# Kernel tuning notes

Measured on AMD Instinct MI355X. Metric: run time of the kernel, lower is better.

Reference implementation:

```python
import jax, jax.numpy as jnp
import numpy as np

D = 64      # in_features
U = 1024    # hidden units
B = 4096    # batch

def _build_masks():
    d0 = np.arange(D)
    dh = np.arange(U) % (D - 1)
    m0 = (d0[None, :] <= dh[:, None]).astype(np.float32)          # [U, D]
    m1 = (dh[None, :] <= dh[:, None]).astype(np.float32)          # [U, U]
    m2 = np.tile((dh[None, :] < d0[:, None]).astype(np.float32), (2, 1))  # [2D, U]
    return jnp.asarray(m0), jnp.asarray(m1), jnp.asarray(m2)


def setup_inputs() -> dict:
    key = jax.random.key(0)
    ks = jax.random.split(key, 7)
    scale = 0.02  # small init so exp(sigma) stays finite
    return {
        "u": jax.random.normal(ks[0], (B, D), dtype=jnp.float32),
        "W0": jax.random.normal(ks[1], (U, D), dtype=jnp.float32) * scale,
        "b0": jax.random.normal(ks[2], (U,), dtype=jnp.float32) * scale,
        "W1": jax.random.normal(ks[3], (U, U), dtype=jnp.float32) * scale,
        "b1": jax.random.normal(ks[4], (U,), dtype=jnp.float32) * scale,
        "W2": jax.random.normal(ks[5], (2 * D, U), dtype=jnp.float32) * scale,
        "b2": jax.random.normal(ks[6], (2 * D,), dtype=jnp.float32) * scale,
    }


def reference(u, W0, b0, W1, b1, W2, b2):
    m0, m1, m2 = _build_masks()
    mW0, mW1, mW2 = m0 * W0, m1 * W1, m2 * W2  # masked weights (constant across steps)

    def made(x):  # x: [B, D] -> mu, sigma each [B, D]
        h = jax.nn.relu(x @ mW0.T + b0)
        h = jax.nn.relu(h @ mW1.T + b1)
        z = h @ mW2.T + b2
        return z[:, :D], z[:, D:]

    def step(carry, i):
        x, ldj = carry
        mu, sigma = made(x)
        # ordering = arange(D) (sequential, not reversed) => idx == i
        x = x.at[:, i].set(u[:, i] * jnp.exp(sigma[:, i]) + mu[:, i])
        ldj = ldj.at[:, i].set(sigma[:, i])
        return (x, ldj), None

    x0 = jnp.zeros_like(u)
    ldj0 = jnp.zeros_like(u)
    (x, ldj), _ = jax.lax.scan(step, (x0, ldj0), jnp.arange(D))
    log_det_jacobian = jnp.sum(ldj, axis=1, keepdims=True)  # [B, 1]
    return x, log_det_jacobian
```

## Files before the change

### kernel.cpp

```cpp
#include <hip/hip_runtime.h>
#include <hip/hip_bf16.h>

#define BATCH 4096
#define NTHR 512

typedef __attribute__((ext_vector_type(8))) short bf16x8;
typedef __attribute__((ext_vector_type(4))) float f32x4;
typedef __attribute__((ext_vector_type(4))) short short4v;

#define BAR() asm volatile("s_waitcnt lgkmcnt(0)\n\ts_barrier" ::: "memory")

__host__ __device__ __forceinline__ int off1(int g) { return (g <= 16) ? 17 * g : 16 * g + 16; }
__host__ __device__ __forceinline__ int cntg(int g) { return (g < 16) ? 17 : 16; }
__host__ __device__ __forceinline__ int unitOf(int p) {
    int gp, jp;
    if (p < 272) { gp = p / 17; jp = p - gp * 17; }
    else         { gp = (p >> 4) - 1; jp = p & 15; }
    return gp + 63 * jp;
}
__device__ __forceinline__ short f2bf(float f) {
    __hip_bfloat16 h = __float2bfloat16(f);
    return *reinterpret_cast<short*>(&h);
}

__global__ void prep7(const float* __restrict__ W0, const float* __restrict__ b0,
                      const float* __restrict__ W1, const float* __restrict__ b1,
                      const float* __restrict__ W2,
                      short* __restrict__ W1f, short* __restrict__ W2f,
                      short* __restrict__ W0f, float* __restrict__ b1p) {
    __shared__ short ws[16][1032];
    const int b = blockIdx.x, t = threadIdx.x;
    if (b < 72) {
        const bool isW1 = (b < 64);
        const int n = t >> 5;
        int u;
        if (isW1) u = unitOf(b * 16 + n);
        else { const int c = b - 64; u = (n & 1) ? (64 + c * 8 + (n >> 1)) : (c * 8 + (n >> 1)); }
        const float* src = isW1 ? (W1 + (long)u * 1024) : (W2 + (long)u * 1024);
        const int c0 = (t & 31) * 4;
#pragma unroll
        for (int j = 0; j < 8; ++j) {
            int c = c0 + j * 128;
            float4 v = *(const float4*)&src[c];
            short4v sv;
            sv[0] = f2bf(v.x); sv[1] = f2bf(v.y); sv[2] = f2bf(v.z); sv[3] = f2bf(v.w);
            *(short4v*)&ws[n][c] = sv;
        }
        __syncthreads();
#pragma unroll 1
        for (int it = 0; it < 8; ++it) {
            int v = t + it * 512;
            if (v < 4032) {
                int g = v >> 6, lane2 = v & 63;
                int nn = lane2 & 15, aq2 = lane2 >> 4;
                bf16x8 pk;
#pragma unroll
                for (int e = 0; e < 8; ++e) {
                    int k = aq2 * 8 + e;
                    pk[e] = (k < cntg(g)) ? ws[nn][g + 63 * k] : (short)0;
                }
                if (isW1) *(bf16x8*)&W1f[(((long)g * 64 + b) * 64 + lane2) * 8] = pk;
                else      *(bf16x8*)&W2f[(((long)g * 8 + (b - 64)) * 64 + lane2) * 8] = pk;
            }
        }
    } else if (b < 88) {
        const int bb = b - 72;
#pragma unroll 1
        for (int j = 0; j < 16; ++j) {
            int q = t + j * 512;
            if (q < 8064) {
                int idx = bb * 8064 + q;
                int g = idx >> 11, rem = idx & 2047;
                int n2 = rem >> 10, kt = (rem >> 9) & 1, lane2 = (rem >> 3) & 63, e = rem & 7;
                int sl = n2 * 16 + (lane2 & 15);
                int kp = kt * 32 + ((lane2 >> 4) << 3) + e;
                float val = 0.f;
                if (sl < cntg(g)) {
                    int u = unitOf(off1(g) + sl);
                    if (kp == 0) val = b0[u];
                    else if (kp - 1 <= g) val = W0[u * 64 + kp - 1];
                }
                W0f[idx] = f2bf(val);
            }
        }
    } else {
        for (int p = t; p < 1024; p += 512) b1p[p] = b1[unitOf(p)];
    }
}

__global__ __launch_bounds__(NTHR, 2) void made7(
    const float* __restrict__ uin, const float* __restrict__ b2,
    const short* __restrict__ W1f, const short* __restrict__ W2f,
    const short* __restrict__ W0f, const float* __restrict__ b1p,
    float* __restrict__ out) {

    __shared__ __align__(16) short h1b[2][16][40];
    __shared__ __align__(16) short h2b[2][16][40];
    __shared__ __align__(16) short xhist[16][80];
    __shared__ __align__(16) float uT[64][16];
    __shared__ __align__(16) float xLs[16][68];
    __shared__ float ldjpart[8][16];

    const int t = threadIdx.x, lane = t & 63, wv = t >> 6;
    const int n = lane & 15, aq = lane >> 4;
    const int rowbase = blockIdx.x * 16;

    {
        int* z1 = (int*)&h1b[0][0][0];
        for (int idx = t; idx < 2 * 16 * 40 / 2; idx += NTHR) z1[idx] = 0;
        int* z2 = (int*)&h2b[0][0][0];
        for (int idx = t; idx < 2 * 16 * 40 / 2; idx += NTHR) z2[idx] = 0;
        int* z3 = (int*)&xhist[0][0];
        for (int idx = t; idx < 16 * 80 / 2; idx += NTHR) z3[idx] = 0;
    }
    if (t < 256) {
        int r = t >> 4, c0 = (t & 15) * 4;
        float4 v = *(const float4*)&uin[(long)(rowbase + r) * 64 + c0];
        uT[c0 + 0][r] = v.x; uT[c0 + 1][r] = v.y; uT[c0 + 2][r] = v.z; uT[c0 + 3][r] = v.w;
    }

    const int B = (wv == 0) ? 0 : (wv == 1) ? 7 : (wv == 2) ? 15 : 8 * wv;
    const int C = (wv == 1 || wv == 2) ? 9 : 8;

    f32x4 acc2[9];
#pragma unroll
    for (int s = 0; s < 9; ++s) {
        float bb = (s < C) ? b1p[(B + s) * 16 + n] : 0.f;
        acc2[s] = (f32x4){bb, bb, bb, bb};
    }
    f32x4 zacc;
    {
        int pc = wv * 16 + n;
        float bz = b2[(pc >> 1) + 64 * (pc & 1)];
        zacc = (f32x4){bz, bz, bz, bz};
    }

    bf16x8 w1f[9], w2g, w2gm1, w0f0, w0f1, w0f2;
#pragma unroll
    for (int s = 0; s < 9; ++s)
        if (s < C)
            w1f[s] = *(const bf16x8*)&W1f[(((long)0 * 64 + (B + s)) * 64 + lane) * 8];
    w2g = *(const bf16x8*)&W2f[(((long)0 * 8 + wv) * 64 + lane) * 8];
    w2gm1 = w2g;
    {
        const long gb = 8 * wv;
        w0f0 = *(const bf16x8*)&W0f[((gb * 4 + 0) * 64 + lane) * 8];
        w0f1 = *(const bf16x8*)&W0f[((gb * 4 + 1) * 64 + lane) * 8];
        w0f2 = *(const bf16x8*)&W0f[((gb * 4 + 2) * 64 + lane) * 8];
    }

    f32x4 ldjacc = {0.f, 0.f, 0.f, 0.f};
    BAR();
    if (t < 16) xhist[t][0] = (short)0x3F80;
    float ureg[4];
#pragma unroll
    for (int r = 0; r < 4; ++r) ureg[r] = uT[8 * wv + (n >> 1)][aq * 4 + r];

#pragma unroll 1
    for (int i = 0; i < 64; ++i) {
        const int g = i - 1;
        const bool isPub = (wv == (i >> 3));

        if (g >= 0) {
            const int og = off1(g);
            const int tf0 = og >> 4;
            const bf16x8 af1 = *(const bf16x8*)&h1b[(i + 1) & 1][n][aq * 8];
            const int s0 = tf0 - B;
#pragma unroll
            for (int s = 0; s < 9; ++s)
                if (s < C && s >= s0)
                    acc2[s] = __builtin_amdgcn_mfma_f32_16x16x32_bf16(af1, w1f[s], acc2[s], 0, 0, 0);
            {
                const int gp = (i < 63) ? i : 62;
                const int s0p = (off1(gp) >> 4) - B;
#pragma unroll
                for (int s = 0; s < 9; ++s)
                    if (s < C && s >= s0p)
                        w1f[s] = *(const bf16x8*)&W1f[(((long)gp * 64 + (B + s)) * 64 + lane) * 8];
            }
            const bool freshedPrev = (wv == ((i - 1) >> 3));
            if (!isPub && !freshedPrev && g >= 1) {
                const bf16x8 af2p = *(const bf16x8*)&h2b[(i - 1) & 1][n][aq * 8];
                zacc = __builtin_amdgcn_mfma_f32_16x16x32_bf16(af2p, w2gm1, zacc, 0, 0, 0);
            }
        }

        if (isPub) {
            if (g >= 0) {
                const int og = off1(g), cg = cntg(g);
                const int tf0 = og >> 4, tfl = (og + cg - 1) >> 4;
                if ((i & 7) == 0 && g >= 1) {
                    const bf16x8 af2p = *(const bf16x8*)&h2b[(i - 1) & 1][n][aq * 8];
                    zacc = __builtin_amdgcn_mfma_f32_16x16x32_bf16(af2p, w2gm1, zacc, 0, 0, 0);
                }
                {
                    const int sT = tf0 - B;
                    const int j = tf0 * 16 + n - og;
                    if (j >= 0 && j < cg) {
#pragma unroll
                        for (int r = 0; r < 4; ++r) {
                            float v = acc2[sT][r];
                            h2b[i & 1][aq * 4 + r][j] = f2bf(v > 0.f ? v : 0.f);
                        }
                    }
                }
                if (tfl != tf0) {
                    const int sT = tfl - B;
                    const int j = tfl * 16 + n - og;
                    if (j < cg) {
#pragma unroll
                        for (int r = 0; r < 4; ++r) {
                            float v = acc2[sT][r];
                            h2b[i & 1][aq * 4 + r][j] = f2bf(v > 0.f ? v : 0.f);
                        }
                    }
                }
                if ((g == 16 || g == 17) && n == 0) {
#pragma unroll
                    for (int r = 0; r < 4; ++r) h2b[i & 1][aq * 4 + r][16] = 0;
                }
                const bf16x8 af2 = *(const bf16x8*)&h2b[i & 1][n][aq * 8];
                zacc = __builtin_amdgcn_mfma_f32_16x16x32_bf16(af2, w2g, zacc, 0, 0, 0);
            }
            {
                const int n0 = 2 * (i & 7);
                f32x4 sgv;
#pragma unroll
                for (int r = 0; r < 4; ++r) sgv[r] = __shfl_xor(zacc[r], 1);
                if (n == n0) {
#pragma unroll
                    for (int r = 0; r < 4; ++r) {
                        const float sg = sgv[r], mu = zacc[r];
                        const float x = ureg[r] * __expf(sg) + mu;
                        ldjacc[r] += sg;
                        const int m = aq * 4 + r;
                        xLs[m][i] = x;
                        if (i < 63) xhist[m][i + 1] = f2bf(x);
                    }
                }
            }
            if (i < 63) {
                const bf16x8 ax0 = *(const bf16x8*)&xhist[n][aq * 8];
                f32x4 d0 = {0.f, 0.f, 0.f, 0.f};
                d0 = __builtin_amdgcn_mfma_f32_16x16x32_bf16(ax0, w0f0, d0, 0, 0, 0);
                if (i >= 31) {
                    const bf16x8 ax1 = *(const bf16x8*)&xhist[n][32 + aq * 8];
                    d0 = __builtin_amdgcn_mfma_f32_16x16x32_bf16(ax1, w0f1, d0, 0, 0, 0);
                }
                f32x4 d1 = {0.f, 0.f, 0.f, 0.f};
                if (i < 16)
                    d1 = __builtin_amdgcn_mfma_f32_16x16x32_bf16(ax0, w0f2, d1, 0, 0, 0);
#pragma unroll
                for (int r = 0; r < 4; ++r) {
                    float v = d0[r];
                    h1b[i & 1][aq * 4 + r][n] = f2bf(v > 0.f ? v : 0.f);
                }
                if (n == 0) {
#pragma unroll
                    for (int r = 0; r < 4; ++r) {
                        float v = (i < 16) ? (d1[r] > 0.f ? d1[r] : 0.f) : 0.f;
                        h1b[i & 1][aq * 4 + r][16] = f2bf(v);
                    }
                }
                if (i + 1 < 63 && ((i + 1) >> 3) == wv) {
                    const long gb = i + 1;
                    w0f0 = *(const bf16x8*)&W0f[((gb * 4 + 0) * 64 + lane) * 8];
                    w0f1 = *(const bf16x8*)&W0f[((gb * 4 + 1) * 64 + lane) * 8];
                    w0f2 = *(const bf16x8*)&W0f[((gb * 4 + 2) * 64 + lane) * 8];
                }
            }
        }

        w2gm1 = w2g;
        {
            const int gz = (i < 63) ? i : 62;
            w2g = *(const bf16x8*)&W2f[(((long)gz * 8 + wv) * 64 + lane) * 8];
        }
        BAR();
    }

#pragma unroll
    for (int r = 0; r < 4; ++r) {
        float v = ldjacc[r];
        v += __shfl_xor(v, 2);
        v += __shfl_xor(v, 4);
        v += __shfl_xor(v, 8);
        if (n == 0) ldjpart[wv][aq * 4 + r] = v;
    }
    BAR();

    if (t < 256) {
        int r = t >> 4, c = (t & 15) * 4;
        float4 v;
        v.x = xLs[r][c]; v.y = xLs[r][c + 1]; v.z = xLs[r][c + 2]; v.w = xLs[r][c + 3];
        *(float4*)&out[(long)(rowbase + r) * 64 + c] = v;
    }
    if (t < 16) {
        float s = 0.f;
#pragma unroll
        for (int w = 0; w < 8; ++w) s += ldjpart[w][t];
        out[(long)BATCH * 64 + rowbase + t] = s;
    }
}

extern "C" void kernel_launch(void* const* d_in, const int* in_sizes, int n_in,
                              void* d_out, int out_size, void* d_ws, size_t ws_size,
                              hipStream_t stream) {
    (void)in_sizes; (void)n_in; (void)out_size; (void)ws_size;
    const float* u  = (const float*)d_in[0];
    const float* W0 = (const float*)d_in[1];
    const float* b0 = (const float*)d_in[2];
    const float* W1 = (const float*)d_in[3];
    const float* b1 = (const float*)d_in[4];
    const float* W2 = (const float*)d_in[5];
    const float* b2 = (const float*)d_in[6];
    float* out = (float*)d_out;

    short* W1f = (short*)d_ws;
    short* W2f = (short*)((char*)d_ws + 4128768);
    short* W0f = (short*)((char*)d_ws + 4128768 + 516096);
    float* b1p = (float*)((char*)d_ws + 4128768 + 516096 + 258048);

    prep7<<<dim3(89), dim3(512), 0, stream>>>(W0, b0, W1, b1, W2, W1f, W2f, W0f, b1p);
    made7<<<dim3(BATCH / 16), dim3(NTHR), 0, stream>>>(u, b2, W1f, W2f, W0f, b1p, out);
}
```

Before: 212.6 us.

## Defer bulk MFMA accumulation by several steps and barrier every fourth iteration

The per-step layer-1 and layer-2 history buffers become 8-slot rings. Non-publishing waves now accumulate contributions several steps late, while the publishing wave patches in the most recent few steps itself with extra MFMAs using freshly loaded weight shards. This lets the block-wide barrier run only every fourth step instead of every step, cutting synchronisation on the serial 64-step chain. The cost is redundant MFMAs and extra weight loads on the critical wave, more LDS, and dropping the occupancy hint from launch_bounds.

```diff
diff --git a/kernel.cpp b/kernel.cpp
--- a/kernel.cpp
+++ b/kernel.cpp
@@ -23,7 +23,7 @@
     return *reinterpret_cast<short*>(&h);
 }
 
-__global__ void prep7(const float* __restrict__ W0, const float* __restrict__ b0,
+__global__ void prep9(const float* __restrict__ W0, const float* __restrict__ b0,
                       const float* __restrict__ W1, const float* __restrict__ b1,
                       const float* __restrict__ W2,
                       short* __restrict__ W1f, short* __restrict__ W2f,
@@ -88,14 +88,14 @@
     }
 }
 
-__global__ __launch_bounds__(NTHR, 2) void made7(
+__global__ __launch_bounds__(NTHR) void made9(
     const float* __restrict__ uin, const float* __restrict__ b2,
     const short* __restrict__ W1f, const short* __restrict__ W2f,
     const short* __restrict__ W0f, const float* __restrict__ b1p,
     float* __restrict__ out) {
 
-    __shared__ __align__(16) short h1b[2][16][40];
-    __shared__ __align__(16) short h2b[2][16][40];
+    __shared__ __align__(16) short h1r[8][16][40];
+    __shared__ __align__(16) short h2r[8][16][40];
     __shared__ __align__(16) short xhist[16][80];
     __shared__ __align__(16) float uT[64][16];
     __shared__ __align__(16) float xLs[16][68];
@@ -106,10 +106,10 @@
     const int rowbase = blockIdx.x * 16;
 
     {
-        int* z1 = (int*)&h1b[0][0][0];
-        for (int idx = t; idx < 2 * 16 * 40 / 2; idx += NTHR) z1[idx] = 0;
-        int* z2 = (int*)&h2b[0][0][0];
-        for (int idx = t; idx < 2 * 16 * 40 / 2; idx += NTHR) z2[idx] = 0;
+        int* z1 = (int*)&h1r[0][0][0];
+        for (int idx = t; idx < 8 * 16 * 40 / 2; idx += NTHR) z1[idx] = 0;
+        int* z2 = (int*)&h2r[0][0][0];
+        for (int idx = t; idx < 8 * 16 * 40 / 2; idx += NTHR) z2[idx] = 0;
         int* z3 = (int*)&xhist[0][0];
         for (int idx = t; idx < 16 * 80 / 2; idx += NTHR) z3[idx] = 0;
     }
@@ -135,20 +135,22 @@
         zacc = (f32x4){bz, bz, bz, bz};
     }
 
-    bf16x8 w1f[9], w2g, w2gm1, w0f0, w0f1, w0f2;
+    bf16x8 w1f[9];
+    bf16x8 w2a, w2b, w2c, w2d, w2e;
+    bf16x8 shA0, shA1, shA2, shB0, shB1, shB2;
+    bf16x8 w0f0, w0f1, w0f2;
 #pragma unroll
     for (int s = 0; s < 9; ++s)
         if (s < C)
             w1f[s] = *(const bf16x8*)&W1f[(((long)0 * 64 + (B + s)) * 64 + lane) * 8];
-    w2g = *(const bf16x8*)&W2f[(((long)0 * 8 + wv) * 64 + lane) * 8];
-    w2gm1 = w2g;
+    w2a = w2b = w2c = w2d = w2e = *(const bf16x8*)&W2f[(((long)0 * 8 + wv) * 64 + lane) * 8];
+    shA0 = shA1 = shA2 = shB0 = shB1 = shB2 = w2a;
     {
         const long gb = 8 * wv;
         w0f0 = *(const bf16x8*)&W0f[((gb * 4 + 0) * 64 + lane) * 8];
         w0f1 = *(const bf16x8*)&W0f[((gb * 4 + 1) * 64 + lane) * 8];
         w0f2 = *(const bf16x8*)&W0f[((gb * 4 + 2) * 64 + lane) * 8];
     }
-
     f32x4 ldjacc = {0.f, 0.f, 0.f, 0.f};
     BAR();
     if (t < 16) xhist[t][0] = (short)0x3F80;
@@ -161,76 +163,104 @@
         const int g = i - 1;
         const bool isPub = (wv == (i >> 3));
 
-        if (g >= 0) {
-            const int og = off1(g);
-            const int tf0 = og >> 4;
-            const bf16x8 af1 = *(const bf16x8*)&h1b[(i + 1) & 1][n][aq * 8];
-            const int s0 = tf0 - B;
+        const int gl = i - 4;
+        if (gl >= 0) {
+            const bf16x8 af1 = *(const bf16x8*)&h1r[gl & 7][n][aq * 8];
+            const int s0 = (off1(gl) >> 4) - B;
 #pragma unroll
             for (int s = 0; s < 9; ++s)
                 if (s < C && s >= s0)
                     acc2[s] = __builtin_amdgcn_mfma_f32_16x16x32_bf16(af1, w1f[s], acc2[s], 0, 0, 0);
-            {
-                const int gp = (i < 63) ? i : 62;
-                const int s0p = (off1(gp) >> 4) - B;
-#pragma unroll
-                for (int s = 0; s < 9; ++s)
-                    if (s < C && s >= s0p)
-                        w1f[s] = *(const bf16x8*)&W1f[(((long)gp * 64 + (B + s)) * 64 + lane) * 8];
-            }
-            const bool freshedPrev = (wv == ((i - 1) >> 3));
-            if (!isPub && !freshedPrev && g >= 1) {
-                const bf16x8 af2p = *(const bf16x8*)&h2b[(i - 1) & 1][n][aq * 8];
-                zacc = __builtin_amdgcn_mfma_f32_16x16x32_bf16(af2p, w2gm1, zacc, 0, 0, 0);
-            }
+        }
+        {
+            const int gp = (i - 3 < 0) ? 0 : ((i - 3 > 62) ? 62 : (i - 3));
+            const int s0p = (off1(gp) >> 4) - B;
+#pragma unroll
+            for (int s = 0; s < 9; ++s)
+                if (s < C && s >= s0p)
+                    w1f[s] = *(const bf16x8*)&W1f[(((long)gp * 64 + (B + s)) * 64 + lane) * 8];
+        }
+        const int gz = i - 5;
+        if (gz >= 0) {
+            const bf16x8 af2 = *(const bf16x8*)&h2r[gz & 7][n][aq * 8];
+            zacc = __builtin_amdgcn_mfma_f32_16x16x32_bf16(af2, w2a, zacc, 0, 0, 0);
         }
 
         if (isPub) {
+            f32x4 ztmp = zacc;
             if (g >= 0) {
                 const int og = off1(g), cg = cntg(g);
                 const int tf0 = og >> 4, tfl = (og + cg - 1) >> 4;
-                if ((i & 7) == 0 && g >= 1) {
-                    const bf16x8 af2p = *(const bf16x8*)&h2b[(i - 1) & 1][n][aq * 8];
-                    zacc = __builtin_amdgcn_mfma_f32_16x16x32_bf16(af2p, w2gm1, zacc, 0, 0, 0);
-                }
+                const int q0 = (g - 2 < 0) ? 0 : (g - 2), q1 = (g - 1 < 0) ? 0 : (g - 1);
+                const bf16x8 h1a = *(const bf16x8*)&h1r[q0 & 7][n][aq * 8];
+                const bf16x8 h1b = *(const bf16x8*)&h1r[q1 & 7][n][aq * 8];
+                const bf16x8 h1c = *(const bf16x8*)&h1r[g & 7][n][aq * 8];
                 {
                     const int sT = tf0 - B;
+                    f32x4 t0 = acc2[0];
+#pragma unroll
+                    for (int s = 1; s < 9; ++s) t0 = (s == sT) ? acc2[s] : t0;
+                    if (g >= 2) t0 = __builtin_amdgcn_mfma_f32_16x16x32_bf16(h1a, shA0, t0, 0, 0, 0);
+                    if (g >= 1) t0 = __builtin_amdgcn_mfma_f32_16x16x32_bf16(h1b, shA1, t0, 0, 0, 0);
+                    t0 = __builtin_amdgcn_mfma_f32_16x16x32_bf16(h1c, shA2, t0, 0, 0, 0);
                     const int j = tf0 * 16 + n - og;
                     if (j >= 0 && j < cg) {
 #pragma unroll
                         for (int r = 0; r < 4; ++r) {
-                            float v = acc2[sT][r];
-                            h2b[i & 1][aq * 4 + r][j] = f2bf(v > 0.f ? v : 0.f);
+                            float v = t0[r];
+                            h2r[g & 7][aq * 4 + r][j] = f2bf(v > 0.f ? v : 0.f);
                         }
                     }
                 }
                 if (tfl != tf0) {
                     const int sT = tfl - B;
+                    f32x4 t1 = acc2[0];
+#pragma unroll
+                    for (int s = 1; s < 9; ++s) t1 = (s == sT) ? acc2[s] : t1;
+                    if (g >= 2) t1 = __builtin_amdgcn_mfma_f32_16x16x32_bf16(h1a, shB0, t1, 0, 0, 0);
+                    if (g >= 1) t1 = __builtin_amdgcn_mfma_f32_16x16x32_bf16(h1b, shB1, t1, 0, 0, 0);
+                    t1 = __builtin_amdgcn_mfma_f32_16x16x32_bf16(h1c, shB2, t1, 0, 0, 0);
                     const int j = tfl * 16 + n - og;
                     if (j < cg) {
 #pragma unroll
                         for (int r = 0; r < 4; ++r) {
-                            float v = acc2[sT][r];
-                            h2b[i & 1][aq * 4 + r][j] = f2bf(v > 0.f ? v : 0.f);
+                            float v = t1[r];
+                            h2r[g & 7][aq * 4 + r][j] = f2bf(v > 0.f ? v : 0.f);
                         }
                     }
                 }
-                if ((g == 16 || g == 17) && n == 0) {
-#pragma unroll
-                    for (int r = 0; r < 4; ++r) h2b[i & 1][aq * 4 + r][16] = 0;
-                }
-                const bf16x8 af2 = *(const bf16x8*)&h2b[i & 1][n][aq * 8];
-                zacc = __builtin_amdgcn_mfma_f32_16x16x32_bf16(af2, w2g, zacc, 0, 0, 0);
+                if (g >= 16 && g < 24 && n == 0) {
+#pragma unroll
+                    for (int r = 0; r < 4; ++r) h2r[g & 7][aq * 4 + r][16] = 0;
+                }
+                const int z0 = (g - 3 < 0) ? 0 : (g - 3), z1 = (g - 2 < 0) ? 0 : (g - 2);
+                const int z2 = (g - 1 < 0) ? 0 : (g - 1);
+                if (g >= 3) {
+                    const bf16x8 a = *(const bf16x8*)&h2r[z0 & 7][n][aq * 8];
+                    ztmp = __builtin_amdgcn_mfma_f32_16x16x32_bf16(a, w2b, ztmp, 0, 0, 0);
+                }
+                if (g >= 2) {
+                    const bf16x8 a = *(const bf16x8*)&h2r[z1 & 7][n][aq * 8];
+                    ztmp = __builtin_amdgcn_mfma_f32_16x16x32_bf16(a, w2c, ztmp, 0, 0, 0);
+                }
+                if (g >= 1) {
+                    const bf16x8 a = *(const bf16x8*)&h2r[z2 & 7][n][aq * 8];
+                    ztmp = __builtin_amdgcn_mfma_f32_16x16x32_bf16(a, w2d, ztmp, 0, 0, 0);
+                }
+                {
+                    const bf16x8 a = *(const bf16x8*)&h2r[g & 7][n][aq * 8];
+                    ztmp = __builtin_amdgcn_mfma_f32_16x16x32_bf16(a, w2e, ztmp, 0, 0, 0);
+                }
             }
             {
                 const int n0 = 2 * (i & 7);
                 f32x4 sgv;
 #pragma unroll
-                for (int r = 0; r < 4; ++r) sgv[r] = __shfl_xor(zacc[r], 1);
+                for (int r = 0; r < 4; ++r) sgv[r] = __shfl_xor(ztmp[r], 1);
                 if (n == n0) {
 #pragma unroll
                     for (int r = 0; r < 4; ++r) {
-                        const float sg = sgv[r], mu = zacc[r];
+                        const float sg = sgv[r], mu = ztmp[r];
                         const float x = ureg[r] * __expf(sg) + mu;
                         ldjacc[r] += sg;
                         const int m = aq * 4 + r;
@@ -253,13 +283,13 @@
 #pragma unroll
                 for (int r = 0; r < 4; ++r) {
                     float v = d0[r];
-                    h1b[i & 1][aq * 4 + r][n] = f2bf(v > 0.f ? v : 0.f);
+                    h1r[i & 7][aq * 4 + r][n] = f2bf(v > 0.f ? v : 0.f);
                 }
                 if (n == 0) {
 #pragma unroll
                     for (int r = 0; r < 4; ++r) {
                         float v = (i < 16) ? (d1[r] > 0.f ? d1[r] : 0.f) : 0.f;
-                        h1b[i & 1][aq * 4 + r][16] = f2bf(v);
+                        h1r[i & 7][aq * 4 + r][16] = f2bf(v);
                     }
                 }
                 if (i + 1 < 63 && ((i + 1) >> 3) == wv) {
@@ -271,12 +301,25 @@
             }
         }
 
-        w2gm1 = w2g;
+        if (i < 63 && ((i + 1) >> 3) == wv) {
+            const int gN = i;
+            const int ogN = off1(gN), cgN = cntg(gN);
+            const int TA = ogN >> 4, TB = (ogN + cgN - 1) >> 4;
+            const int q0 = (gN - 2 < 0) ? 0 : (gN - 2), q1 = (gN - 1 < 0) ? 0 : (gN - 1);
+            shA0 = *(const bf16x8*)&W1f[(((long)q0 * 64 + TA) * 64 + lane) * 8];
+            shA1 = *(const bf16x8*)&W1f[(((long)q1 * 64 + TA) * 64 + lane) * 8];
+            shA2 = *(const bf16x8*)&W1f[(((long)gN * 64 + TA) * 64 + lane) * 8];
+            shB0 = *(const bf16x8*)&W1f[(((long)q0 * 64 + TB) * 64 + lane) * 8];
+            shB1 = *(const bf16x8*)&W1f[(((long)q1 * 64 + TB) * 64 + lane) * 8];
+            shB2 = *(const bf16x8*)&W1f[(((long)gN * 64 + TB) * 64 + lane) * 8];
+        }
+        w2a = w2b; w2b = w2c; w2c = w2d; w2d = w2e;
         {
-            const int gz = (i < 63) ? i : 62;
-            w2g = *(const bf16x8*)&W2f[(((long)gz * 8 + wv) * 64 + lane) * 8];
-        }
-        BAR();
+            const int gw = (i > 62) ? 62 : i;
+            w2e = *(const bf16x8*)&W2f[(((long)gw * 8 + wv) * 64 + lane) * 8];
+        }
+
+        if ((i & 3) == 3) BAR();
     }
 
 #pragma unroll
@@ -321,6 +364,6 @@
     short* W0f = (short*)((char*)d_ws + 4128768 + 516096);
     float* b1p = (float*)((char*)d_ws + 4128768 + 516096 + 258048);
 
-    prep7<<<dim3(89), dim3(512), 0, stream>>>(W0, b0, W1, b1, W2, W1f, W2f, W0f, b1p);
-    made7<<<dim3(BATCH / 16), dim3(NTHR), 0, stream>>>(u, b2, W1f, W2f, W0f, b1p, out);
-}
+    prep9<<<dim3(89), dim3(512), 0, stream>>>(W0, b0, W1, b1, W2, W1f, W2f, W0f, b1p);
+    made9<<<dim3(BATCH / 16), dim3(NTHR), 0, stream>>>(u, b2, W1f, W2f, W0f, b1p, out);
+}
```

Result: faster. 202.6 us (-4.7%).
